# Kernel tuning notes

Measured on AMD Instinct MI355X. Metric: run time of the kernel, lower is better.

## Reference

```python
import jax, jax.numpy as jnp
import numpy as np

B, L, IN_DIM, OUT_DIM = 8, 128, 512, 512
DEP_NUM, DEP_DIM = 45, 16


def setup_inputs() -> dict:
    key = jax.random.key(0)
    ks = jax.random.split(key, 10)
    h = jax.random.normal(ks[0], (B, L, IN_DIM), dtype=jnp.float32)
    dep_type_matrix = jax.random.randint(ks[1], (B, L, L), 0, DEP_NUM, dtype=jnp.int32)
    aspect_mask = jnp.zeros((B, L), dtype=bool).at[:, 10:14].set(True)
    # params (torch Linear convention: y = x @ W.T + b); xavier-ish scale
    def xavier(k, shape):
        fan_in, fan_out = shape[1], shape[0]
        lim = jnp.sqrt(6.0 / (fan_in + fan_out))
        return jax.random.uniform(k, shape, jnp.float32, -lim, lim)
    emb = jax.random.normal(ks[2], (DEP_NUM, DEP_DIM), dtype=jnp.float32)
    W1 = xavier(ks[3], (OUT_DIM, IN_DIM + DEP_DIM))
    b1 = jnp.zeros((OUT_DIM,), jnp.float32)
    W2 = xavier(ks[4], (OUT_DIM, IN_DIM + DEP_DIM))
    b2 = jnp.zeros((OUT_DIM,), jnp.float32)
    Wg = xavier(ks[5], (OUT_DIM, IN_DIM))
    bg = jnp.zeros((OUT_DIM,), jnp.float32)
    bias = jnp.zeros((OUT_DIM,), jnp.float32)
    return {"h": h, "dep_type_matrix": dep_type_matrix, "aspect_mask": aspect_mask,
            "emb": emb, "W1": W1, "b1": b1, "W2": W2, "b2": b2,
            "Wg": Wg, "bg": bg, "bias": bias}


def _position_aware(h, aspect_mask):
    # h: [B,L,D], aspect_mask: [B,L] bool
    Lh = h.shape[1]
    m = aspect_mask.astype(jnp.int32)
    start = jnp.argmax(m, axis=1)                       # first True
    end = Lh - 1 - jnp.argmax(jnp.flip(m, axis=1), axis=1)  # last True
    pos = jnp.arange(Lh)[None, :]                        # [1,L]
    s = start[:, None]
    e = end[:, None]
    inv_L = 1.0 / Lh
    left_w = 1.0 - (s - pos).astype(h.dtype) * inv_L
    right_w = 1.0 - (pos - e).astype(h.dtype) * inv_L
    w = jnp.where(pos < s, left_w, jnp.where(pos > e, right_w, 0.0))
    w = jnp.where(aspect_mask, 0.0, w)                   # zero on aspect words
    return h * w[:, :, None]


def reference(h, dep_type_matrix, aspect_mask, emb, W1, b1, W2, b2, Wg, bg, bias):
    D = h.shape[-1]
    h = _position_aware(h, aspect_mask)
    dep_emb = emb[dep_type_matrix]                       # [B,L,L,E]
    # split concat-linear: W(concat[h_i, e_ij]) = h_i @ Wh.T + e_ij @ Wd.T + b
    W1h, W1d = W1[:, :D], W1[:, D:]
    W2h, W2d = W2[:, :D], W2[:, D:]
    hp_i = jnp.einsum('bid,od->bio', h, W1h)[:, :, None, :] \
        + jnp.einsum('bije,oe->bijo', dep_emb, W1d) + b1   # [B,L,L,O]
    hp_j = jnp.einsum('bid,od->bio', h, W2h)[:, :, None, :] \
        + jnp.einsum('bije,oe->bijo', dep_emb, W2d) + b2   # [B,L,L,O]
    scores = jnp.exp(jnp.sum(hp_i * hp_j, axis=-1))        # [B,L,L]
    adj = (dep_type_matrix != 0).astype(scores.dtype)
    masked = scores * adj
    A = masked / (jnp.sum(masked, axis=-1, keepdims=True) + 1e-6)
    h_trans = jnp.einsum('bid,od->bio', h, Wg) + bg        # [B,L,O]
    out = jnp.einsum('bij,bjo->bio', A, h_trans) + bias
    return jax.nn.relu(out)
```

## Files before the change

kernel.cpp:

```cpp
#include <hip/hip_runtime.h>
#include <hip/hip_bf16.h>
#include <math.h>

#define NBATCH 8
#define NL 128
#define IND 512
#define DEPN 45
#define DEPD 16
#define WCOLS 528
#define NP 1664
#define C_P1 0
#define C_P2 512
#define C_HT 1024
#define C_D1 1536
#define C_D2 1581
#define C_PAD 1626

typedef __attribute__((ext_vector_type(8))) short bf16x8;
typedef __attribute__((ext_vector_type(4))) float f32x4;

__device__ inline ushort f2bf(float x) {
    __hip_bfloat16 b = __float2bfloat16(x);
    return *reinterpret_cast<ushort*>(&b);
}
__device__ inline float bf2f(ushort u) {
    __hip_bfloat16 b;
    *reinterpret_cast<ushort*>(&b) = u;
    return __bfloat162float(b);
}

__global__ __launch_bounds__(256) void k_prep(
    const float* __restrict__ h, const unsigned char* __restrict__ mask,
    const float* __restrict__ emb,
    const float* __restrict__ W1, const float* __restrict__ W2,
    const float* __restrict__ Wg,
    const float* __restrict__ b1, const float* __restrict__ b2,
    const float* __restrict__ bg,
    ushort* __restrict__ A_hi, ushort* __restrict__ A_lo,
    ushort* __restrict__ B_hi, ushort* __restrict__ B_lo,
    float* __restrict__ bias_ext) {
    int bid = blockIdx.x;
    int tid = threadIdx.x;

    if (bid < 64) {
        int rb = bid * 16;
        int b = rb >> 7;
        __shared__ int sflag, smin, smax;
        __shared__ float w16[16];
        if (tid == 0) { sflag = 0; smin = NL; smax = -1; }
        __syncthreads();
        const int* mi = (const int*)mask;
        if (tid < 128) {
            int v0 = mi[tid], v1 = mi[tid + 128];
            if ((unsigned)v0 > 1u || (unsigned)v1 > 1u) atomicOr(&sflag, 1);
        }
        __syncthreads();
        if (tid < 128) {
            int mval = sflag ? (int)mask[b * NL + tid] : mi[b * NL + tid];
            if (mval) { atomicMin(&smin, tid); atomicMax(&smax, tid); }
        }
        __syncthreads();
        if (tid < 16) {
            int any = (smax >= 0);
            int s = any ? smin : 0;
            int e = any ? smax : (NL - 1);
            int i = (rb & 127) + tid;
            const float invL = 1.0f / (float)NL;
            float w;
            if (i < s)      w = 1.0f - (float)(s - i) * invL;
            else if (i > e) w = 1.0f - (float)(i - e) * invL;
            else            w = 0.0f;
            int mval = sflag ? (int)mask[b * NL + i] : mi[b * NL + i];
            if (mval) w = 0.0f;
            w16[tid] = w;
        }
        __syncthreads();
        for (int idx = tid; idx < 16 * 128; idx += 256) {
            int r = idx >> 7, dc = (idx & 127) << 2;
            float4 hv = *(const float4*)&h[(size_t)(rb + r) * IND + dc];
            float wv = w16[r];
            hv.x *= wv; hv.y *= wv; hv.z *= wv; hv.w *= wv;
            ushort4 hi4, lo4;
            hi4.x = f2bf(hv.x); hi4.y = f2bf(hv.y); hi4.z = f2bf(hv.z); hi4.w = f2bf(hv.w);
            lo4.x = f2bf(hv.x - bf2f(hi4.x));
            lo4.y = f2bf(hv.y - bf2f(hi4.y));
            lo4.z = f2bf(hv.z - bf2f(hi4.z));
            lo4.w = f2bf(hv.w - bf2f(hi4.w));
            *(ushort4*)&A_hi[(size_t)(rb + r) * IND + dc] = hi4;
            *(ushort4*)&A_lo[(size_t)(rb + r) * IND + dc] = lo4;
        }
        if (bid == 0) {
            for (int i = tid; i < 512; i += 256) {
                bias_ext[C_P1 + i] = b1[i];
                bias_ext[C_P2 + i] = b2[i];
                bias_ext[C_HT + i] = bg[i];
            }
            if (tid < NP - C_PAD) bias_ext[C_PAD + tid] = 0.f;
        }
    } else if (bid < 160) {
        int nb = (bid - 64) * 16;
        for (int idx = tid; idx < 16 * 128; idx += 256) {
            int r = idx >> 7, dc = (idx & 127) << 2;
            int n = nb + r;
            const float* src;
            if (n < 512)       src = W1 + (size_t)n * WCOLS + dc;
            else if (n < 1024) src = W2 + (size_t)(n - 512) * WCOLS + dc;
            else               src = Wg + (size_t)(n - 1024) * IND + dc;
            float4 wv = *(const float4*)src;
            ushort4 hi4, lo4;
            hi4.x = f2bf(wv.x); hi4.y = f2bf(wv.y); hi4.z = f2bf(wv.z); hi4.w = f2bf(wv.w);
            lo4.x = f2bf(wv.x - bf2f(hi4.x));
            lo4.y = f2bf(wv.y - bf2f(hi4.y));
            lo4.z = f2bf(wv.z - bf2f(hi4.z));
            lo4.w = f2bf(wv.w - bf2f(hi4.w));
            *(ushort4*)&B_hi[(size_t)n * IND + dc] = hi4;
            *(ushort4*)&B_lo[(size_t)n * IND + dc] = lo4;
        }
    } else if (bid < 162) {
        int nb = 1626 + (bid - 160) * 19;
        ushort4 z4 = {0, 0, 0, 0};
        for (int idx = tid; idx < 19 * 128; idx += 256) {
            int r = idx >> 7, dc = (idx & 127) << 2;
            *(ushort4*)&B_hi[(size_t)(nb + r) * IND + dc] = z4;
            *(ushort4*)&B_lo[(size_t)(nb + r) * IND + dc] = z4;
        }
    } else {
        int zi = bid - 162;
        int t = zi % 45;
        int m = (zi / 45) & 1;
        int dq = zi / 90;
        __shared__ float es[DEPD];
        __shared__ float ys[512];
        __shared__ float y1s[512];
        __shared__ float part[256];
        if (tid < DEPD) es[tid] = emb[t * DEPD + tid];
        __syncthreads();
        const float* Wdep = (m == 0) ? W2 : W1;
        for (int o = tid; o < 512; o += 256) {
            float s = 0.f;
#pragma unroll
            for (int e = 0; e < DEPD; e++) s += es[e] * Wdep[o * WCOLS + IND + e];
            ys[o] = s;
        }
        if (m == 0 && dq == 0) {
            for (int o = tid; o < 512; o += 256) {
                float s = 0.f;
#pragma unroll
                for (int e = 0; e < DEPD; e++) s += es[e] * W1[o * WCOLS + IND + e];
                y1s[o] = s;
            }
        }
        __syncthreads();
        int dloc = tid & 127, half = tid >> 7;
        const float* Wsrc = (m == 0) ? W1 : W2;
        int d = dq * 128 + dloc;
        int obase = half * 256;
        float s = 0.f;
#pragma unroll 16
        for (int oo = 0; oo < 256; oo++)
            s += Wsrc[(size_t)(obase + oo) * WCOLS + d] * ys[obase + oo];
        part[tid] = s;
        __syncthreads();
        int row = ((m == 0) ? C_D1 : C_D2) + t;
        if (half == 0) {
            float tot = part[dloc] + part[128 + dloc];
            ushort hi = f2bf(tot);
            B_hi[(size_t)row * IND + d] = hi;
            B_lo[(size_t)row * IND + d] = f2bf(tot - bf2f(hi));
        }
        if (dq == 0 && tid < 64) {
            const float* bb = (m == 0) ? b1 : b2;
            float sb = 0.f;
#pragma unroll
            for (int k = 0; k < 8; k++) sb += bb[tid + k * 64] * ys[tid + k * 64];
            if (m == 0) {
#pragma unroll
                for (int k = 0; k < 8; k++) sb += y1s[tid + k * 64] * ys[tid + k * 64];
            }
            for (int off = 32; off; off >>= 1) sb += __shfl_down(sb, off, 64);
            if (tid == 0) bias_ext[row] = sb;
        }
    }
}

#define LOADSET(P, KS) \
    P##a0h = *(const bf16x8*)(A_hi + (size_t)rA0 * IND + (KS) * 32 + kg8); \
    P##a0l = *(const bf16x8*)(A_lo + (size_t)rA0 * IND + (KS) * 32 + kg8); \
    P##a1h = *(const bf16x8*)(A_hi + (size_t)rA1 * IND + (KS) * 32 + kg8); \
    P##a1l = *(const bf16x8*)(A_lo + (size_t)rA1 * IND + (KS) * 32 + kg8); \
    P##b0h = *(const bf16x8*)(B_hi + (size_t)cB0 * IND + (KS) * 32 + kg8); \
    P##b0l = *(const bf16x8*)(B_lo + (size_t)cB0 * IND + (KS) * 32 + kg8); \
    P##b1h = *(const bf16x8*)(B_hi + (size_t)cB1 * IND + (KS) * 32 + kg8); \
    P##b1l = *(const bf16x8*)(B_lo + (size_t)cB1 * IND + (KS) * 32 + kg8);

#define MFMASET(P) \
    acc00 = __builtin_amdgcn_mfma_f32_16x16x32_bf16(P##a0h, P##b0h, acc00, 0, 0, 0); \
    acc00 = __builtin_amdgcn_mfma_f32_16x16x32_bf16(P##a0h, P##b0l, acc00, 0, 0, 0); \
    acc00 = __builtin_amdgcn_mfma_f32_16x16x32_bf16(P##a0l, P##b0h, acc00, 0, 0, 0); \
    acc01 = __builtin_amdgcn_mfma_f32_16x16x32_bf16(P##a0h, P##b1h, acc01, 0, 0, 0); \
    acc01 = __builtin_amdgcn_mfma_f32_16x16x32_bf16(P##a0h, P##b1l, acc01, 0, 0, 0); \
    acc01 = __builtin_amdgcn_mfma_f32_16x16x32_bf16(P##a0l, P##b1h, acc01, 0, 0, 0); \
    acc10 = __builtin_amdgcn_mfma_f32_16x16x32_bf16(P##a1h, P##b0h, acc10, 0, 0, 0); \
    acc10 = __builtin_amdgcn_mfma_f32_16x16x32_bf16(P##a1h, P##b0l, acc10, 0, 0, 0); \
    acc10 = __builtin_amdgcn_mfma_f32_16x16x32_bf16(P##a1l, P##b0h, acc10, 0, 0, 0); \
    acc11 = __builtin_amdgcn_mfma_f32_16x16x32_bf16(P##a1h, P##b1h, acc11, 0, 0, 0); \
    acc11 = __builtin_amdgcn_mfma_f32_16x16x32_bf16(P##a1h, P##b1l, acc11, 0, 0, 0); \
    acc11 = __builtin_amdgcn_mfma_f32_16x16x32_bf16(P##a1l, P##b1h, acc11, 0, 0, 0);

__global__ __launch_bounds__(128) void k3_gemm(
    const ushort* __restrict__ A_hi, const ushort* __restrict__ A_lo,
    const ushort* __restrict__ B_hi, const ushort* __restrict__ B_lo,
    const float* __restrict__ bias_ext, float* __restrict__ Pout,
    ushort* __restrict__ HTb) {
    int tid = threadIdx.x;
    int wid = tid >> 6, lane = tid & 63;
    int lrow = lane & 15, kg8 = (lane >> 4) << 3;
    int mbase = blockIdx.x * 64 + wid * 32;
    int nbase = blockIdx.y * 32;
    int rA0 = mbase + lrow, rA1 = rA0 + 16;
    int cB0 = nbase + lrow, cB1 = cB0 + 16;

    f32x4 acc00 = {0.f, 0.f, 0.f, 0.f};
    f32x4 acc01 = acc00, acc10 = acc00, acc11 = acc00;
    bf16x8 pa0h, pa0l, pa1h, pa1l, pb0h, pb0l, pb1h, pb1l;
    bf16x8 qa0h, qa0l, qa1h, qa1l, qb0h, qb0l, qb1h, qb1l;

    LOADSET(p, 0)
#pragma unroll
    for (int ks = 0; ks < 16; ks += 2) {
        LOADSET(q, ks + 1)
        MFMASET(p)
        int kn = (ks + 2) & 15;
        LOADSET(p, kn)
        MFMASET(q)
    }

    int r0 = (lane >> 4) << 2;
    int col0 = nbase + lrow;
    int col1 = col0 + 16;
    float bv0 = bias_ext[col0];
    float bv1 = bias_ext[col1];

    if (nbase >= C_HT && nbase < C_HT + 512) {
        int o0 = col0 - C_HT, o1 = col1 - C_HT;
#pragma unroll
        for (int r = 0; r < 4; ++r) {
            int row0 = mbase + r0 + r;
            int row1 = row0 + 16;
            HTb[(size_t)row0 * 512 + o0] = f2bf(acc00[r] + bv0);
            HTb[(size_t)row0 * 512 + o1] = f2bf(acc01[r] + bv1);
            HTb[(size_t)row1 * 512 + o0] = f2bf(acc10[r] + bv0);
            HTb[(size_t)row1 * 512 + o1] = f2bf(acc11[r] + bv1);
        }
    } else {
#pragma unroll
        for (int r = 0; r < 4; ++r) {
            int row0 = mbase + r0 + r;
            int row1 = row0 + 16;
            Pout[(size_t)row0 * NP + col0] = acc00[r] + bv0;
            Pout[(size_t)row0 * NP + col1] = acc01[r] + bv1;
            Pout[(size_t)row1 * NP + col0] = acc10[r] + bv0;
            Pout[(size_t)row1 * NP + col1] = acc11[r] + bv1;
        }
    }
}

__global__ __launch_bounds__(128) void k5_out(
    const float* __restrict__ P, const int* __restrict__ dep,
    const ushort* __restrict__ HTb, const float* __restrict__ bias,
    float* __restrict__ out) {
    int row = blockIdx.x;
    int b = row >> 7;
    int tid = threadIdx.x;
    __shared__ float comb[DEPN];
    __shared__ float a[NL];
    __shared__ float red[2];
    __shared__ float sumv;

    const float* Prow = P + (size_t)row * NP;
    float4 p1 = *(const float4*)(Prow + C_P1 + tid * 4);
    float4 p2 = *(const float4*)(Prow + C_P2 + tid * 4);
    float lc = p1.x * p2.x + p1.y * p2.y + p1.z * p2.z + p1.w * p2.w;
    for (int off = 32; off; off >>= 1) lc += __shfl_down(lc, off, 64);
    if ((tid & 63) == 0) red[tid >> 6] = lc;
    if (tid < DEPN) comb[tid] = Prow[C_D1 + tid] + Prow[C_D2 + tid];
    __syncthreads();

    float c0 = red[0] + red[1];
    int tt = dep[(size_t)row * NL + tid];
    float sc = (tt != 0) ? expf(c0 + comb[tt]) : 0.f;
    a[tid] = sc;
    __syncthreads();
    if (tid < 64) {
        float v = a[tid] + a[tid + 64];
        for (int off = 32; off; off >>= 1) v += __shfl_down(v, off, 64);
        if (tid == 0) sumv = v;
    }
    __syncthreads();
    float inv = 1.0f / (sumv + 1e-6f);
    if (tid < NL) a[tid] *= inv;
    __syncthreads();

    const ushort* htb = HTb + (size_t)b * NL * 512 + tid * 4;
    float sx = 0.f, sy = 0.f, sz = 0.f, sw = 0.f;
#pragma unroll 8
    for (int j = 0; j < NL; j += 2) {
        float a0 = a[j], a1 = a[j + 1];
        ushort4 v0 = *(const ushort4*)(htb + (size_t)j * 512);
        ushort4 v1 = *(const ushort4*)(htb + (size_t)(j + 1) * 512);
        sx += a0 * bf2f(v0.x) + a1 * bf2f(v1.x);
        sy += a0 * bf2f(v0.y) + a1 * bf2f(v1.y);
        sz += a0 * bf2f(v0.z) + a1 * bf2f(v1.z);
        sw += a0 * bf2f(v0.w) + a1 * bf2f(v1.w);
    }
    float4 bv = *(const float4*)&bias[tid * 4];
    float4 o;
    o.x = fmaxf(sx + bv.x, 0.f);
    o.y = fmaxf(sy + bv.y, 0.f);
    o.z = fmaxf(sz + bv.z, 0.f);
    o.w = fmaxf(sw + bv.w, 0.f);
    *(float4*)&out[(size_t)row * 512 + tid * 4] = o;
}

extern "C" void kernel_launch(void* const* d_in, const int* in_sizes, int n_in,
                              void* d_out, int out_size, void* d_ws, size_t ws_size,
                              hipStream_t stream) {
    const float* h    = (const float*)d_in[0];
    const int* dep    = (const int*)d_in[1];
    const unsigned char* mask = (const unsigned char*)d_in[2];
    const float* emb  = (const float*)d_in[3];
    const float* W1   = (const float*)d_in[4];
    const float* b1   = (const float*)d_in[5];
    const float* W2   = (const float*)d_in[6];
    const float* b2   = (const float*)d_in[7];
    const float* Wg   = (const float*)d_in[8];
    const float* bg   = (const float*)d_in[9];
    const float* bias = (const float*)d_in[10];
    float* out = (float*)d_out;

    char* p = (char*)d_ws;
    ushort* A_hi = (ushort*)p;  p += (size_t)1024 * 512 * 2;
    ushort* A_lo = (ushort*)p;  p += (size_t)1024 * 512 * 2;
    ushort* B_hi = (ushort*)p;  p += (size_t)NP * 512 * 2;
    ushort* B_lo = (ushort*)p;  p += (size_t)NP * 512 * 2;
    ushort* HTb = (ushort*)p;   p += (size_t)1024 * 512 * 2;
    float* bias_ext = (float*)p; p += NP * 4;
    float* Pout = (float*)p;

    k_prep<<<522, 256, 0, stream>>>(h, mask, emb, W1, W2, Wg, b1, b2, bg,
                                    A_hi, A_lo, B_hi, B_lo, bias_ext);
    dim3 g3(16, 52);
    k3_gemm<<<g3, 128, 0, stream>>>(A_hi, A_lo, B_hi, B_lo, bias_ext, Pout, HTb);
    k5_out<<<NBATCH * NL, 128, 0, stream>>>(Pout, dep, HTb, bias, out);
}
```

Before: 57.73 us.

## Stage GEMM operands through LDS via global_load_lds and retile blocks

The split-bf16 GEMM kernel previously loaded A and B fragments directly from global memory into registers per wave. It now copies 128-wide K chunks of A/B hi/lo into shared memory using async global-to-LDS loads and has both waves read their fragments from LDS. Block tiling changes from 64x32 to 32x64 so the two waves share the A tile. The intent is to cut redundant global traffic and get wide coalesced loads, at the cost of barrier synchronisation with no double buffering, which exposes load latency in each chunk.

```diff
diff --git a/kernel.cpp b/kernel.cpp
--- a/kernel.cpp
+++ b/kernel.cpp
@@ -27,6 +27,12 @@
     __hip_bfloat16 b;
     *reinterpret_cast<ushort*>(&b) = u;
     return __bfloat162float(b);
+}
+
+__device__ __forceinline__ void gl16(const ushort* g, ushort* l) {
+    __builtin_amdgcn_global_load_lds(
+        (const __attribute__((address_space(1))) unsigned int*)g,
+        (__attribute__((address_space(3))) unsigned int*)l, 16, 0, 0);
 }
 
 __global__ __launch_bounds__(256) void k_prep(
@@ -183,30 +189,6 @@
     }
 }
 
-#define LOADSET(P, KS) \
-    P##a0h = *(const bf16x8*)(A_hi + (size_t)rA0 * IND + (KS) * 32 + kg8); \
-    P##a0l = *(const bf16x8*)(A_lo + (size_t)rA0 * IND + (KS) * 32 + kg8); \
-    P##a1h = *(const bf16x8*)(A_hi + (size_t)rA1 * IND + (KS) * 32 + kg8); \
-    P##a1l = *(const bf16x8*)(A_lo + (size_t)rA1 * IND + (KS) * 32 + kg8); \
-    P##b0h = *(const bf16x8*)(B_hi + (size_t)cB0 * IND + (KS) * 32 + kg8); \
-    P##b0l = *(const bf16x8*)(B_lo + (size_t)cB0 * IND + (KS) * 32 + kg8); \
-    P##b1h = *(const bf16x8*)(B_hi + (size_t)cB1 * IND + (KS) * 32 + kg8); \
-    P##b1l = *(const bf16x8*)(B_lo + (size_t)cB1 * IND + (KS) * 32 + kg8);
-
-#define MFMASET(P) \
-    acc00 = __builtin_amdgcn_mfma_f32_16x16x32_bf16(P##a0h, P##b0h, acc00, 0, 0, 0); \
-    acc00 = __builtin_amdgcn_mfma_f32_16x16x32_bf16(P##a0h, P##b0l, acc00, 0, 0, 0); \
-    acc00 = __builtin_amdgcn_mfma_f32_16x16x32_bf16(P##a0l, P##b0h, acc00, 0, 0, 0); \
-    acc01 = __builtin_amdgcn_mfma_f32_16x16x32_bf16(P##a0h, P##b1h, acc01, 0, 0, 0); \
-    acc01 = __builtin_amdgcn_mfma_f32_16x16x32_bf16(P##a0h, P##b1l, acc01, 0, 0, 0); \
-    acc01 = __builtin_amdgcn_mfma_f32_16x16x32_bf16(P##a0l, P##b1h, acc01, 0, 0, 0); \
-    acc10 = __builtin_amdgcn_mfma_f32_16x16x32_bf16(P##a1h, P##b0h, acc10, 0, 0, 0); \
-    acc10 = __builtin_amdgcn_mfma_f32_16x16x32_bf16(P##a1h, P##b0l, acc10, 0, 0, 0); \
-    acc10 = __builtin_amdgcn_mfma_f32_16x16x32_bf16(P##a1l, P##b0h, acc10, 0, 0, 0); \
-    acc11 = __builtin_amdgcn_mfma_f32_16x16x32_bf16(P##a1h, P##b1h, acc11, 0, 0, 0); \
-    acc11 = __builtin_amdgcn_mfma_f32_16x16x32_bf16(P##a1h, P##b1l, acc11, 0, 0, 0); \
-    acc11 = __builtin_amdgcn_mfma_f32_16x16x32_bf16(P##a1l, P##b1h, acc11, 0, 0, 0);
-
 __global__ __launch_bounds__(128) void k3_gemm(
     const ushort* __restrict__ A_hi, const ushort* __restrict__ A_lo,
     const ushort* __restrict__ B_hi, const ushort* __restrict__ B_lo,
@@ -214,34 +196,83 @@
     ushort* __restrict__ HTb) {
     int tid = threadIdx.x;
     int wid = tid >> 6, lane = tid & 63;
-    int lrow = lane & 15, kg8 = (lane >> 4) << 3;
-    int mbase = blockIdx.x * 64 + wid * 32;
-    int nbase = blockIdx.y * 32;
-    int rA0 = mbase + lrow, rA1 = rA0 + 16;
-    int cB0 = nbase + lrow, cB1 = cB0 + 16;
+    int lrow = lane & 15;
+    int mbase = blockIdx.x * 32;
+    int nbase = blockIdx.y * 64;
+
+    __shared__ ushort Ah[16 * 32 * 8];
+    __shared__ ushort Al[16 * 32 * 8];
+    __shared__ ushort Bh[16 * 64 * 8];
+    __shared__ ushort Bl[16 * 64 * 8];
+
+    const ushort* aSrcH = A_hi + (size_t)(mbase + (lane & 31)) * IND + ((lane >> 5) << 3);
+    const ushort* aSrcL = A_lo + (size_t)(mbase + (lane & 31)) * IND + ((lane >> 5) << 3);
+    const ushort* bSrcH = B_hi + (size_t)(nbase + lane) * IND;
+    const ushort* bSrcL = B_lo + (size_t)(nbase + lane) * IND;
+
+#define STAGE(C) { \
+    int ck = (C) * 128; \
+    if (wid == 0) { \
+        _Pragma("unroll") \
+        for (int i = 0; i < 8; i++) gl16(aSrcH + ck + (i << 4), &Ah[i << 9]); \
+        _Pragma("unroll") \
+        for (int i = 0; i < 8; i++) gl16(aSrcL + ck + (i << 4), &Al[i << 9]); \
+        _Pragma("unroll") \
+        for (int g = 0; g < 8; g++) gl16(bSrcH + ck + (g << 3), &Bh[g << 9]); \
+    } else { \
+        _Pragma("unroll") \
+        for (int g = 8; g < 16; g++) gl16(bSrcH + ck + (g << 3), &Bh[g << 9]); \
+        _Pragma("unroll") \
+        for (int g = 0; g < 16; g++) gl16(bSrcL + ck + (g << 3), &Bl[g << 9]); \
+    } }
 
     f32x4 acc00 = {0.f, 0.f, 0.f, 0.f};
     f32x4 acc01 = acc00, acc10 = acc00, acc11 = acc00;
-    bf16x8 pa0h, pa0l, pa1h, pa1l, pb0h, pb0l, pb1h, pb1l;
-    bf16x8 qa0h, qa0l, qa1h, qa1l, qb0h, qb0l, qb1h, qb1l;
-
-    LOADSET(p, 0)
-#pragma unroll
-    for (int ks = 0; ks < 16; ks += 2) {
-        LOADSET(q, ks + 1)
-        MFMASET(p)
-        int kn = (ks + 2) & 15;
-        LOADSET(p, kn)
-        MFMASET(q)
-    }
+
+    STAGE(0)
+    for (int c = 0; c < 4; c++) {
+        __syncthreads();
+#pragma unroll
+        for (int KS = 0; KS < 4; KS++) {
+            int gl = (KS << 2) + (lane >> 4);
+            int ga = ((gl << 5) + lrow) << 3;
+            int gb = ((gl << 6) + (wid << 5) + lrow) << 3;
+            bf16x8 a0h = *(const bf16x8*)&Ah[ga];
+            bf16x8 a0l = *(const bf16x8*)&Al[ga];
+            bf16x8 a1h = *(const bf16x8*)&Ah[ga + 128];
+            bf16x8 a1l = *(const bf16x8*)&Al[ga + 128];
+            bf16x8 b0h = *(const bf16x8*)&Bh[gb];
+            bf16x8 b0l = *(const bf16x8*)&Bl[gb];
+            bf16x8 b1h = *(const bf16x8*)&Bh[gb + 128];
+            bf16x8 b1l = *(const bf16x8*)&Bl[gb + 128];
+            acc00 = __builtin_amdgcn_mfma_f32_16x16x32_bf16(a0h, b0h, acc00, 0, 0, 0);
+            acc00 = __builtin_amdgcn_mfma_f32_16x16x32_bf16(a0h, b0l, acc00, 0, 0, 0);
+            acc00 = __builtin_amdgcn_mfma_f32_16x16x32_bf16(a0l, b0h, acc00, 0, 0, 0);
+            acc01 = __builtin_amdgcn_mfma_f32_16x16x32_bf16(a0h, b1h, acc01, 0, 0, 0);
+            acc01 = __builtin_amdgcn_mfma_f32_16x16x32_bf16(a0h, b1l, acc01, 0, 0, 0);
+            acc01 = __builtin_amdgcn_mfma_f32_16x16x32_bf16(a0l, b1h, acc01, 0, 0, 0);
+            acc10 = __builtin_amdgcn_mfma_f32_16x16x32_bf16(a1h, b0h, acc10, 0, 0, 0);
+            acc10 = __builtin_amdgcn_mfma_f32_16x16x32_bf16(a1h, b0l, acc10, 0, 0, 0);
+            acc10 = __builtin_amdgcn_mfma_f32_16x16x32_bf16(a1l, b0h, acc10, 0, 0, 0);
+            acc11 = __builtin_amdgcn_mfma_f32_16x16x32_bf16(a1h, b1h, acc11, 0, 0, 0);
+            acc11 = __builtin_amdgcn_mfma_f32_16x16x32_bf16(a1h, b1l, acc11, 0, 0, 0);
+            acc11 = __builtin_amdgcn_mfma_f32_16x16x32_bf16(a1l, b1h, acc11, 0, 0, 0);
+        }
+        if (c < 3) {
+            __syncthreads();
+            STAGE(c + 1)
+        }
+    }
+#undef STAGE
 
     int r0 = (lane >> 4) << 2;
-    int col0 = nbase + lrow;
+    int colb = nbase + (wid << 5);
+    int col0 = colb + lrow;
     int col1 = col0 + 16;
     float bv0 = bias_ext[col0];
     float bv1 = bias_ext[col1];
 
-    if (nbase >= C_HT && nbase < C_HT + 512) {
+    if (colb >= C_HT && colb < C_HT + 512) {
         int o0 = col0 - C_HT, o1 = col1 - C_HT;
 #pragma unroll
         for (int r = 0; r < 4; ++r) {
@@ -349,7 +380,7 @@
 
     k_prep<<<522, 256, 0, stream>>>(h, mask, emb, W1, W2, Wg, b1, b2, bg,
                                     A_hi, A_lo, B_hi, B_lo, bias_ext);
-    dim3 g3(16, 52);
+    dim3 g3(32, 26);
     k3_gemm<<<g3, 128, 0, stream>>>(A_hi, A_lo, B_hi, B_lo, bias_ext, Pout, HTb);
     k5_out<<<NBATCH * NL, 128, 0, stream>>>(Pout, dep, HTb, bias, out);
 }
```

Result: faster. 55.93 us (-3.1%).
